# Optimization experiments

Measured on AMD Instinct MI355X. Metric: run time of the kernel, lower is better.

Reference implementation:

```python
import jax, jax.numpy as jnp
import numpy as np

N = 100000
E = 6400000
NT_DIM = 8
HID = 32


def setup_inputs() -> dict:
    key = jax.random.key(0)
    k1, k2, k3, k4, k5, k6, k7 = jax.random.split(key, 7)
    nt_emb = jax.random.normal(k1, (N, NT_DIM), dtype=jnp.float32)
    edge_index = jax.random.randint(k2, (2, E), 0, N, dtype=jnp.int64)
    lm_mask = jax.random.uniform(k3, (N,), dtype=jnp.float32)
    fan_in1 = 2 * NT_DIM + 2
    lim1 = 1.0 / np.sqrt(fan_in1)
    W1 = jax.random.uniform(k4, (fan_in1, HID), minval=-lim1, maxval=lim1, dtype=jnp.float32)
    b1 = jax.random.uniform(k5, (HID,), minval=-lim1, maxval=lim1, dtype=jnp.float32)
    lim2 = 1.0 / np.sqrt(HID)
    W2 = jax.random.uniform(k6, (HID, 1), minval=-lim2, maxval=lim2, dtype=jnp.float32)
    b2 = jax.random.uniform(k7, (1,), minval=-lim2, maxval=lim2, dtype=jnp.float32)
    return {"nt_emb": nt_emb, "edge_index": edge_index, "lm_mask": lm_mask,
            "W1": W1, "b1": b1, "W2": W2, "b2": b2}


def reference(nt_emb, edge_index, lm_mask, W1, b1, W2, b2):
    s, d = edge_index[0], edge_index[1]
    # [E, 2*nt_dim + 2] edge features: src emb, dst emb, src mask, dst mask
    feat = jnp.concatenate(
        [nt_emb[s], nt_emb[d], lm_mask[s][:, None], lm_mask[d][:, None]], axis=-1)
    h = jax.nn.relu(feat @ W1 + b1)          # [E, hid]
    out = jax.nn.sigmoid(h @ W2 + b2)        # [E, 1]
    return out[:, 0]                         # [E]
```

## Files before the change

### kernel.cpp

```cpp
#include <hip/hip_runtime.h>
#include <hip/hip_bf16.h>

typedef short short8 __attribute__((ext_vector_type(8)));
typedef float floatx4 __attribute__((ext_vector_type(4)));
typedef float floatx16 __attribute__((ext_vector_type(16)));

#define HID 32
#define NTD 8
#define FAN_IN 18

__device__ __forceinline__ short f2bf(float f) {
    union { float f; unsigned u; } v; v.f = f;
    unsigned r = v.u + 0x7fffu + ((v.u >> 16) & 1u);
    return (short)(r >> 16);
}

__device__ __forceinline__ unsigned short pack_emb(float f, unsigned bit) {
    union { float f; unsigned u; } v; v.f = f;
    unsigned r = v.u + 0xFFFFu + ((v.u >> 17) & 1u);
    unsigned short s = (unsigned short)((r >> 16) & 0xFFFEu);
    return (unsigned short)(s | bit);
}

__device__ __forceinline__ float fast_sigmoid(float x) {
    float e = __builtin_amdgcn_exp2f(x * -1.44269504f);
    return __builtin_amdgcn_rcpf(1.0f + e);
}

__global__ void build_table(const float* __restrict__ emb,
                            const float* __restrict__ mask,
                            unsigned short* __restrict__ T, int N) {
    int n = blockIdx.x * blockDim.x + threadIdx.x;
    if (n >= N) return;
    const float4* p = (const float4*)(emb + (size_t)n * NTD);
    float4 lo = p[0], hi = p[1];
    float ev[8] = {lo.x, lo.y, lo.z, lo.w, hi.x, hi.y, hi.z, hi.w};
    float mf = mask[n] * 255.0f + 0.5f;
    unsigned m8 = (unsigned)mf; if (m8 > 255u) m8 = 255u;
    unsigned short row[8];
    #pragma unroll
    for (int j = 0; j < 8; ++j)
        row[j] = pack_emb(ev[j], (m8 >> j) & 1u);
    int4 out;
    out.x = (int)((unsigned)row[0] | ((unsigned)row[1] << 16));
    out.y = (int)((unsigned)row[2] | ((unsigned)row[3] << 16));
    out.z = (int)((unsigned)row[4] | ((unsigned)row[5] << 16));
    out.w = (int)((unsigned)row[6] | ((unsigned)row[7] << 16));
    *(int4*)(T + (size_t)n * 8) = out;
}

__device__ __forceinline__ unsigned decode_m8(int4 r) {
    unsigned m;
    m  = ((unsigned)r.x & 1u);
    m |= (((unsigned)r.x >> 16) & 1u) << 1;
    m |= ((unsigned)r.y & 1u) << 2;
    m |= (((unsigned)r.y >> 16) & 1u) << 3;
    m |= ((unsigned)r.z & 1u) << 4;
    m |= (((unsigned)r.z >> 16) & 1u) << 5;
    m |= ((unsigned)r.w & 1u) << 6;
    m |= (((unsigned)r.w >> 16) & 1u) << 7;
    return m;
}


template <int ESZ>
__device__ __forceinline__ uint2 ld_idx2(const char* __restrict__ idxBase,
                                         unsigned grp, unsigned nGroups,
                                         unsigned E, unsigned cc) {
    unsigned g = grp < nGroups ? grp : nGroups - 1u;
    unsigned eA = g * 64u + cc;
    unsigned eB = eA + 32u;
    if (eA >= E) eA = E - 1u;
    if (eB >= E) eB = E - 1u;
    uint2 r;
    r.x = *(const unsigned*)(idxBase + (size_t)eA * ESZ);
    r.y = *(const unsigned*)(idxBase + (size_t)eB * ESZ);
    return r;
}

__device__ __forceinline__ int4 grow(const char* __restrict__ Tc, unsigned idx) {
    return *(const int4*)(Tc + (size_t)idx * 16u);
}

__device__ __forceinline__ void tile_frags(int4 row, int h, short8& fb1, short8& fb2) {
    unsigned m8 = decode_m8(row);
    unsigned m8p = (unsigned)__shfl_xor((int)m8, 32, 64);
    float mfv = (float)m8p * (1.0f / 255.0f);
    unsigned mbf = (unsigned)(unsigned short)f2bf(mfv);
    int4 b1i, b2i;
    if (h) {
        b1i.x = (int)(mbf | 0x3F800000u);
        b1i.y = 0; b1i.z = 0; b1i.w = 0;
        b2i = row;
    } else {
        b1i = row;
        b2i.x = (int)mbf;
        b2i.y = 0; b2i.z = 0; b2i.w = 0;
    }
    fb1 = __builtin_bit_cast(short8, b1i);
    fb2 = __builtin_bit_cast(short8, b2i);
}

template <int ESZ>
__device__ void run32(const char* __restrict__ ei,
                      const char* __restrict__ Tc,
                      float* __restrict__ out, unsigned E,
                      short8 as, short8 ad, const float* __restrict__ w2r, float bias2,
                      unsigned waveId, unsigned nWaves, int h, int c, int lane) {
    const unsigned nGroups = (E + 63u) >> 6;
    const char* idxBase = ei + (h ? (size_t)E * ESZ : 0);
    const unsigned cc = (unsigned)c;

    if (waveId >= nGroups) return;
    unsigned cur = waveId;

    uint2 i0 = ld_idx2<ESZ>(idxBase, cur, nGroups, E, cc);
    int4 rA = grow(Tc, i0.x);
    int4 rB = grow(Tc, i0.y);
    uint2 i1 = ld_idx2<ESZ>(idxBase, cur + nWaves, nGroups, E, cc);

    while (true) {
        int4 nA = grow(Tc, i1.x);
        int4 nB = grow(Tc, i1.y);
        uint2 i2 = ld_idx2<ESZ>(idxBase, cur + 2u * nWaves, nGroups, E, cc);

        short8 fb1A, fb2A, fb1B, fb2B;
        tile_frags(rA, h, fb1A, fb2A);
        tile_frags(rB, h, fb1B, fb2B);

        floatx16 accA = {0.f,0.f,0.f,0.f,0.f,0.f,0.f,0.f,0.f,0.f,0.f,0.f,0.f,0.f,0.f,0.f};
        floatx16 accB = accA;
        accA = __builtin_amdgcn_mfma_f32_32x32x16_bf16(as, fb1A, accA, 0, 0, 0);
        accB = __builtin_amdgcn_mfma_f32_32x32x16_bf16(as, fb1B, accB, 0, 0, 0);
        accA = __builtin_amdgcn_mfma_f32_32x32x16_bf16(ad, fb2A, accA, 0, 0, 0);
        accB = __builtin_amdgcn_mfma_f32_32x32x16_bf16(ad, fb2B, accB, 0, 0, 0);

        float pA0 = 0.f, pA1 = 0.f, pB0 = 0.f, pB1 = 0.f;
        #pragma unroll
        for (int q = 0; q < 16; q += 2) {
            pA0 += fmaxf(accA[q],     0.f) * w2r[q];
            pA1 += fmaxf(accA[q + 1], 0.f) * w2r[q + 1];
            pB0 += fmaxf(accB[q],     0.f) * w2r[q];
            pB1 += fmaxf(accB[q + 1], 0.f) * w2r[q + 1];
        }
        float pA = pA0 + pA1;
        float pB = pB0 + pB1;
        pA += __shfl_xor(pA, 32, 64);
        pB += __shfl_xor(pB, 32, 64);
        float vA = fast_sigmoid(pA + bias2);
        float vB = fast_sigmoid(pB + bias2);

        float v = (h == 0) ? vA : vB;
        unsigned e = (cur << 6) + (unsigned)lane;
        if (e < E) out[e] = v;

        cur += nWaves;
        if (cur >= nGroups) break;
        rA = nA; rB = nB;
        i1 = i2;
    }
}

__global__ __launch_bounds__(256, 4) void lg_table_kernel(
    const char* __restrict__ ei_bytes,
    const unsigned short* __restrict__ T,
    const float* __restrict__ W1,
    const float* __restrict__ b1,
    const float* __restrict__ W2,
    const float* __restrict__ b2,
    float* __restrict__ out,
    long long E)
{
    const int lane = threadIdx.x & 63;
    const int waveInBlock = threadIdx.x >> 6;
    const unsigned waveId = (unsigned)(blockIdx.x * (blockDim.x >> 6) + waveInBlock);
    const unsigned nWaves = (unsigned)(gridDim.x * (blockDim.x >> 6));

    const int* ei32 = (const int*)ei_bytes;
    int probe = ei32[2 * lane + 1];
    unsigned long long nz = __ballot(probe != 0);
    const int esz = (nz == 0ull) ? 8 : 4;

    const int c = lane & 31;
    const int h = lane >> 5;

    short8 as, ad;
    #pragma unroll
    for (int j = 0; j < 8; ++j) {
        float vs = 0.f, vd = 0.f;
        if (h == 0) {
            vs = W1[j * HID + c];
            if (j == 0) vd = W1[17 * HID + c];
        } else {
            if (j == 0) vs = W1[16 * HID + c];
            else if (j == 1) vs = b1[c];
            vd = W1[(8 + j) * HID + c];
        }
        as[j] = f2bf(vs);
        ad[j] = f2bf(vd);
    }

    float w2r[16];
    #pragma unroll
    for (int q = 0; q < 16; ++q)
        w2r[q] = W2[(q & 3) + 8 * (q >> 2) + 4 * h];

    const float bias2 = b2[0];

    if (esz == 8)
        run32<8>(ei_bytes, (const char*)T, out, (unsigned)E, as, ad, w2r, bias2,
                 waveId, nWaves, h, c, lane);
    else
        run32<4>(ei_bytes, (const char*)T, out, (unsigned)E, as, ad, w2r, bias2,
                 waveId, nWaves, h, c, lane);
}

__global__ __launch_bounds__(256, 4) void lg_kernel(
    const float* __restrict__ nt_emb,
    const char* __restrict__ ei_bytes,
    const float* __restrict__ lm_mask,
    const float* __restrict__ W1,
    const float* __restrict__ b1,
    const float* __restrict__ W2,
    const float* __restrict__ b2,
    float* __restrict__ out,
    long long E)
{
    const int lane = threadIdx.x & 63;
    const int waveInBlock = threadIdx.x >> 6;
    const long long waveId = (long long)blockIdx.x * (blockDim.x >> 6) + waveInBlock;
    const long long nWaves = (long long)gridDim.x * (blockDim.x >> 6);

    const int* ei32 = (const int*)ei_bytes;
    int probe = ei32[2 * lane + 1];
    unsigned long long nz = __ballot(probe != 0);
    const long long esz = (nz == 0ull) ? 8 : 4;

    const int r = lane & 15;
    const int g = lane >> 4;

    short8 a0, a1;
    #pragma unroll
    for (int j = 0; j < 8; ++j) {
        int k = g * 8 + j;
        float v0 = 0.f, v1 = 0.f;
        if (k < FAN_IN)       { v0 = W1[k * HID + r];      v1 = W1[k * HID + 16 + r]; }
        else if (k == FAN_IN) { v0 = b1[r];                v1 = b1[16 + r]; }
        a0[j] = f2bf(v0);
        a1[j] = f2bf(v1);
    }

    float w2v0[4], w2v1[4];
    #pragma unroll
    for (int q = 0; q < 4; ++q) {
        w2v0[q] = W2[g * 4 + q];
        w2v1[q] = W2[16 + g * 4 + q];
    }
    const float bias2 = b2[0];

    const long long nGroups = (E + 15) >> 4;
    for (long long grp = waveId; grp < nGroups; grp += nWaves) {
        long long e = (grp << 4) + r;
        const bool valid = (e < E);
        long long ec = valid ? e : (E - 1);

        int s = *(const int*)(ei_bytes + ec * esz);
        int d = *(const int*)(ei_bytes + (E + ec) * esz);

        short8 fb;
        #pragma unroll
        for (int j = 0; j < 8; ++j) fb[j] = 0;
        if (g < 2) {
            const float4* p = (const float4*)(nt_emb + (long long)(g == 0 ? s : d) * NTD);
            float4 lo = p[0];
            float4 hi = p[1];
            fb[0] = f2bf(lo.x); fb[1] = f2bf(lo.y); fb[2] = f2bf(lo.z); fb[3] = f2bf(lo.w);
            fb[4] = f2bf(hi.x); fb[5] = f2bf(hi.y); fb[6] = f2bf(hi.z); fb[7] = f2bf(hi.w);
        } else if (g == 2) {
            fb[0] = f2bf(lm_mask[s]);
            fb[1] = f2bf(lm_mask[d]);
            fb[2] = (short)0x3F80;
        }

        floatx4 acc0 = {0.f, 0.f, 0.f, 0.f};
        floatx4 acc1 = {0.f, 0.f, 0.f, 0.f};
        acc0 = __builtin_amdgcn_mfma_f32_16x16x32_bf16(a0, fb, acc0, 0, 0, 0);
        acc1 = __builtin_amdgcn_mfma_f32_16x16x32_bf16(a1, fb, acc1, 0, 0, 0);

        float partial = 0.f;
        #pragma unroll
        for (int q = 0; q < 4; ++q) {
            partial += fmaxf(acc0[q], 0.f) * w2v0[q];
            partial += fmaxf(acc1[q], 0.f) * w2v1[q];
        }
        partial += __shfl_xor(partial, 16, 64);
        partial += __shfl_xor(partial, 32, 64);

        float val = fast_sigmoid(partial + bias2);
        if (g == 0 && valid) out[e] = val;
    }
}

extern "C" void kernel_launch(void* const* d_in, const int* in_sizes, int n_in,
                              void* d_out, int out_size, void* d_ws, size_t ws_size,
                              hipStream_t stream) {
    const float* nt_emb = (const float*)d_in[0];
    const char*  ei     = (const char*)d_in[1];
    const float* lm     = (const float*)d_in[2];
    const float* W1     = (const float*)d_in[3];
    const float* b1     = (const float*)d_in[4];
    const float* W2     = (const float*)d_in[5];
    const float* b2     = (const float*)d_in[6];
    float* out = (float*)d_out;

    long long E = (long long)in_sizes[1] / 2;
    int N = in_sizes[2];

    size_t tableBytes = (size_t)N * 16;
    if (ws_size >= tableBytes) {
        unsigned short* T = (unsigned short*)d_ws;
        build_table<<<dim3((N + 255) / 256), dim3(256), 0, stream>>>(nt_emb, lm, T, N);
        lg_table_kernel<<<dim3(2048), dim3(256), 0, stream>>>(ei, T, W1, b1, W2, b2, out, E);
    } else {
        lg_kernel<<<dim3(2048), dim3(256), 0, stream>>>(nt_emb, ei, lm, W1, b1, W2, b2, out, E);
    }
}
```

Measured before the change: 74.51 us.

## Launch one wave per edge group and precompute weight fragments in table build

```diff
diff --git a/kernel.cpp b/kernel.cpp
--- a/kernel.cpp
+++ b/kernel.cpp
@@ -29,8 +29,47 @@
 
 __global__ void build_table(const float* __restrict__ emb,
                             const float* __restrict__ mask,
+                            const float* __restrict__ W1,
+                            const float* __restrict__ b1,
+                            const float* __restrict__ W2,
+                            const float* __restrict__ b2,
                             unsigned short* __restrict__ T, int N) {
     int n = blockIdx.x * blockDim.x + threadIdx.x;
+
+    if (blockIdx.x == 0 && threadIdx.x < 64) {
+        int t = threadIdx.x;
+        int c = t & 31;
+        int h = t >> 5;
+        short8 as, ad;
+        #pragma unroll
+        for (int j = 0; j < 8; ++j) {
+            float vs = 0.f, vd = 0.f;
+            if (h == 0) {
+                vs = W1[j * HID + c];
+                if (j == 0) vd = W1[17 * HID + c];
+            } else {
+                if (j == 0) vs = W1[16 * HID + c];
+                else if (j == 1) vs = b1[c];
+                vd = W1[(8 + j) * HID + c];
+            }
+            as[j] = f2bf(vs);
+            ad[j] = f2bf(vd);
+        }
+        char* aux = (char*)(T + (size_t)N * 8) + (size_t)t * 96;
+        *(short8*)(aux) = as;
+        *(short8*)(aux + 16) = ad;
+        float w2r[16];
+        #pragma unroll
+        for (int q = 0; q < 16; ++q)
+            w2r[q] = W2[(q & 3) + 8 * (q >> 2) + 4 * h];
+        *(float4*)(aux + 32) = *(float4*)(&w2r[0]);
+        *(float4*)(aux + 48) = *(float4*)(&w2r[4]);
+        *(float4*)(aux + 64) = *(float4*)(&w2r[8]);
+        *(float4*)(aux + 80) = *(float4*)(&w2r[12]);
+        if (t == 0)
+            *(float*)((char*)(T + (size_t)N * 8) + 6144) = b2[0];
+    }
+
     if (n >= N) return;
     const float4* p = (const float4*)(emb + (size_t)n * NTD);
     float4 lo = p[0], hi = p[1];
@@ -41,12 +80,12 @@
     #pragma unroll
     for (int j = 0; j < 8; ++j)
         row[j] = pack_emb(ev[j], (m8 >> j) & 1u);
-    int4 out;
-    out.x = (int)((unsigned)row[0] | ((unsigned)row[1] << 16));
-    out.y = (int)((unsigned)row[2] | ((unsigned)row[3] << 16));
-    out.z = (int)((unsigned)row[4] | ((unsigned)row[5] << 16));
-    out.w = (int)((unsigned)row[6] | ((unsigned)row[7] << 16));
-    *(int4*)(T + (size_t)n * 8) = out;
+    int4 o;
+    o.x = (int)((unsigned)row[0] | ((unsigned)row[1] << 16));
+    o.y = (int)((unsigned)row[2] | ((unsigned)row[3] << 16));
+    o.z = (int)((unsigned)row[4] | ((unsigned)row[5] << 16));
+    o.w = (int)((unsigned)row[6] | ((unsigned)row[7] << 16));
+    *(int4*)(T + (size_t)n * 8) = o;
 }
 
 __device__ __forceinline__ unsigned decode_m8(int4 r) {
@@ -60,26 +99,6 @@
     m |= ((unsigned)r.w & 1u) << 6;
     m |= (((unsigned)r.w >> 16) & 1u) << 7;
     return m;
-}
-
-
-template <int ESZ>
-__device__ __forceinline__ uint2 ld_idx2(const char* __restrict__ idxBase,
-                                         unsigned grp, unsigned nGroups,
-                                         unsigned E, unsigned cc) {
-    unsigned g = grp < nGroups ? grp : nGroups - 1u;
-    unsigned eA = g * 64u + cc;
-    unsigned eB = eA + 32u;
-    if (eA >= E) eA = E - 1u;
-    if (eB >= E) eB = E - 1u;
-    uint2 r;
-    r.x = *(const unsigned*)(idxBase + (size_t)eA * ESZ);
-    r.y = *(const unsigned*)(idxBase + (size_t)eB * ESZ);
-    return r;
-}
-
-__device__ __forceinline__ int4 grow(const char* __restrict__ Tc, unsigned idx) {
-    return *(const int4*)(Tc + (size_t)idx * 16u);
 }
 
 __device__ __forceinline__ void tile_frags(int4 row, int h, short8& fb1, short8& fb2) {
@@ -101,80 +120,79 @@
     fb2 = __builtin_bit_cast(short8, b2i);
 }
 
+
 template <int ESZ>
-__device__ void run32(const char* __restrict__ ei,
-                      const char* __restrict__ Tc,
-                      float* __restrict__ out, unsigned E,
-                      short8 as, short8 ad, const float* __restrict__ w2r, float bias2,
-                      unsigned waveId, unsigned nWaves, int h, int c, int lane) {
-    const unsigned nGroups = (E + 63u) >> 6;
+__device__ __forceinline__ void do_group(const char* __restrict__ ei,
+                                         const char* __restrict__ Tc,
+                                         size_t auxOff,
+                                         float* __restrict__ out, unsigned E,
+                                         unsigned grp, int h, int c, int lane) {
     const char* idxBase = ei + (h ? (size_t)E * ESZ : 0);
     const unsigned cc = (unsigned)c;
 
-    if (waveId >= nGroups) return;
-    unsigned cur = waveId;
-
-    uint2 i0 = ld_idx2<ESZ>(idxBase, cur, nGroups, E, cc);
-    int4 rA = grow(Tc, i0.x);
-    int4 rB = grow(Tc, i0.y);
-    uint2 i1 = ld_idx2<ESZ>(idxBase, cur + nWaves, nGroups, E, cc);
-
-    while (true) {
-        int4 nA = grow(Tc, i1.x);
-        int4 nB = grow(Tc, i1.y);
-        uint2 i2 = ld_idx2<ESZ>(idxBase, cur + 2u * nWaves, nGroups, E, cc);
-
-        short8 fb1A, fb2A, fb1B, fb2B;
-        tile_frags(rA, h, fb1A, fb2A);
-        tile_frags(rB, h, fb1B, fb2B);
-
-        floatx16 accA = {0.f,0.f,0.f,0.f,0.f,0.f,0.f,0.f,0.f,0.f,0.f,0.f,0.f,0.f,0.f,0.f};
-        floatx16 accB = accA;
-        accA = __builtin_amdgcn_mfma_f32_32x32x16_bf16(as, fb1A, accA, 0, 0, 0);
-        accB = __builtin_amdgcn_mfma_f32_32x32x16_bf16(as, fb1B, accB, 0, 0, 0);
-        accA = __builtin_amdgcn_mfma_f32_32x32x16_bf16(ad, fb2A, accA, 0, 0, 0);
-        accB = __builtin_amdgcn_mfma_f32_32x32x16_bf16(ad, fb2B, accB, 0, 0, 0);
-
-        float pA0 = 0.f, pA1 = 0.f, pB0 = 0.f, pB1 = 0.f;
-        #pragma unroll
-        for (int q = 0; q < 16; q += 2) {
-            pA0 += fmaxf(accA[q],     0.f) * w2r[q];
-            pA1 += fmaxf(accA[q + 1], 0.f) * w2r[q + 1];
-            pB0 += fmaxf(accB[q],     0.f) * w2r[q];
-            pB1 += fmaxf(accB[q + 1], 0.f) * w2r[q + 1];
-        }
-        float pA = pA0 + pA1;
-        float pB = pB0 + pB1;
-        pA += __shfl_xor(pA, 32, 64);
-        pB += __shfl_xor(pB, 32, 64);
-        float vA = fast_sigmoid(pA + bias2);
-        float vB = fast_sigmoid(pB + bias2);
-
-        float v = (h == 0) ? vA : vB;
-        unsigned e = (cur << 6) + (unsigned)lane;
-        if (e < E) out[e] = v;
-
-        cur += nWaves;
-        if (cur >= nGroups) break;
-        rA = nA; rB = nB;
-        i1 = i2;
-    }
-}
-
-__global__ __launch_bounds__(256, 4) void lg_table_kernel(
+    unsigned eA = grp * 64u + cc;
+    unsigned eB = eA + 32u;
+    if (eA >= E) eA = E - 1u;
+    if (eB >= E) eB = E - 1u;
+    unsigned iA = *(const unsigned*)(idxBase + (size_t)eA * ESZ);
+    unsigned iB = *(const unsigned*)(idxBase + (size_t)eB * ESZ);
+
+    const char* aux = Tc + auxOff + (size_t)lane * 96u;
+    short8 as = *(const short8*)(aux);
+    short8 ad = *(const short8*)(aux + 16);
+    float4 w0 = *(const float4*)(aux + 32);
+    float4 w1v = *(const float4*)(aux + 48);
+    float4 w2v = *(const float4*)(aux + 64);
+    float4 w3v = *(const float4*)(aux + 80);
+    const float bias2 = *(const float*)(Tc + auxOff + 6144);
+
+    int4 rA = *(const int4*)(Tc + (size_t)iA * 16u);
+    int4 rB = *(const int4*)(Tc + (size_t)iB * 16u);
+
+    short8 fb1A, fb2A, fb1B, fb2B;
+    tile_frags(rA, h, fb1A, fb2A);
+    tile_frags(rB, h, fb1B, fb2B);
+
+    floatx16 accA = {0.f,0.f,0.f,0.f,0.f,0.f,0.f,0.f,0.f,0.f,0.f,0.f,0.f,0.f,0.f,0.f};
+    floatx16 accB = accA;
+    accA = __builtin_amdgcn_mfma_f32_32x32x16_bf16(as, fb1A, accA, 0, 0, 0);
+    accB = __builtin_amdgcn_mfma_f32_32x32x16_bf16(as, fb1B, accB, 0, 0, 0);
+    accA = __builtin_amdgcn_mfma_f32_32x32x16_bf16(ad, fb2A, accA, 0, 0, 0);
+    accB = __builtin_amdgcn_mfma_f32_32x32x16_bf16(ad, fb2B, accB, 0, 0, 0);
+
+    float w2r[16] = {w0.x, w0.y, w0.z, w0.w, w1v.x, w1v.y, w1v.z, w1v.w,
+                     w2v.x, w2v.y, w2v.z, w2v.w, w3v.x, w3v.y, w3v.z, w3v.w};
+    float pA0 = 0.f, pA1 = 0.f, pB0 = 0.f, pB1 = 0.f;
+    #pragma unroll
+    for (int q = 0; q < 16; q += 2) {
+        pA0 += fmaxf(accA[q],     0.f) * w2r[q];
+        pA1 += fmaxf(accA[q + 1], 0.f) * w2r[q + 1];
+        pB0 += fmaxf(accB[q],     0.f) * w2r[q];
+        pB1 += fmaxf(accB[q + 1], 0.f) * w2r[q + 1];
+    }
+    float pA = pA0 + pA1;
+    float pB = pB0 + pB1;
+    pA += __shfl_xor(pA, 32, 64);
+    pB += __shfl_xor(pB, 32, 64);
+    float vA = fast_sigmoid(pA + bias2);
+    float vB = fast_sigmoid(pB + bias2);
+
+    float v = (h == 0) ? vA : vB;
+    unsigned e = (grp << 6) + (unsigned)lane;
+    if (e < E) out[e] = v;
+}
+
+__global__ __launch_bounds__(256, 8) void lg_table_kernel(
     const char* __restrict__ ei_bytes,
     const unsigned short* __restrict__ T,
-    const float* __restrict__ W1,
-    const float* __restrict__ b1,
-    const float* __restrict__ W2,
-    const float* __restrict__ b2,
     float* __restrict__ out,
-    long long E)
+    long long E_, int N)
 {
+    const unsigned E = (unsigned)E_;
+    const unsigned nGroups = (E + 63u) >> 6;
     const int lane = threadIdx.x & 63;
-    const int waveInBlock = threadIdx.x >> 6;
-    const unsigned waveId = (unsigned)(blockIdx.x * (blockDim.x >> 6) + waveInBlock);
-    const unsigned nWaves = (unsigned)(gridDim.x * (blockDim.x >> 6));
+    const unsigned waveId = (unsigned)(blockIdx.x * (blockDim.x >> 6) + (threadIdx.x >> 6));
+    if (waveId >= nGroups) return;
 
     const int* ei32 = (const int*)ei_bytes;
     int probe = ei32[2 * lane + 1];
@@ -183,36 +201,12 @@
 
     const int c = lane & 31;
     const int h = lane >> 5;
-
-    short8 as, ad;
-    #pragma unroll
-    for (int j = 0; j < 8; ++j) {
-        float vs = 0.f, vd = 0.f;
-        if (h == 0) {
-            vs = W1[j * HID + c];
-            if (j == 0) vd = W1[17 * HID + c];
-        } else {
-            if (j == 0) vs = W1[16 * HID + c];
-            else if (j == 1) vs = b1[c];
-            vd = W1[(8 + j) * HID + c];
-        }
-        as[j] = f2bf(vs);
-        ad[j] = f2bf(vd);
-    }
-
-    float w2r[16];
-    #pragma unroll
-    for (int q = 0; q < 16; ++q)
-        w2r[q] = W2[(q & 3) + 8 * (q >> 2) + 4 * h];
-
-    const float bias2 = b2[0];
+    const size_t auxOff = (size_t)N * 16u;
 
     if (esz == 8)
-        run32<8>(ei_bytes, (const char*)T, out, (unsigned)E, as, ad, w2r, bias2,
-                 waveId, nWaves, h, c, lane);
+        do_group<8>(ei_bytes, (const char*)T, auxOff, out, E, waveId, h, c, lane);
     else
-        run32<4>(ei_bytes, (const char*)T, out, (unsigned)E, as, ad, w2r, bias2,
-                 waveId, nWaves, h, c, lane);
+        do_group<4>(ei_bytes, (const char*)T, auxOff, out, E, waveId, h, c, lane);
 }
 
 __global__ __launch_bounds__(256, 4) void lg_kernel(
@@ -316,11 +310,14 @@
     long long E = (long long)in_sizes[1] / 2;
     int N = in_sizes[2];
 
-    size_t tableBytes = (size_t)N * 16;
-    if (ws_size >= tableBytes) {
+    size_t needBytes = (size_t)N * 16 + 6144 + 64;
+    if (ws_size >= needBytes) {
         unsigned short* T = (unsigned short*)d_ws;
-        build_table<<<dim3((N + 255) / 256), dim3(256), 0, stream>>>(nt_emb, lm, T, N);
-        lg_table_kernel<<<dim3(2048), dim3(256), 0, stream>>>(ei, T, W1, b1, W2, b2, out, E);
+        build_table<<<dim3((N + 255) / 256), dim3(256), 0, stream>>>(
+            nt_emb, lm, W1, b1, W2, b2, T, N);
+        unsigned nGroups = (unsigned)((E + 63) >> 6);
+        unsigned blocks = (nGroups + 3u) >> 2;
+        lg_table_kernel<<<dim3(blocks), dim3(256), 0, stream>>>(ei, T, out, E, N);
     } else {
         lg_kernel<<<dim3(2048), dim3(256), 0, stream>>>(nt_emb, ei, lm, W1, b1, W2, b2, out, E);
     }
```

After: 76.71 us. +2.9%, slower.
